# Optimization experiments

Measured on AMD Instinct MI355X. Metric: run time of the kernel, lower is better.

The kernel has to match this reference:

```python
import jax, jax.numpy as jnp
import numpy as np

N = 2048
RESTITUTION = 0.5
EPS = 1e-12


def setup_inputs() -> dict:
    key = jax.random.key(0)
    k1, k2, k3, k4 = jax.random.split(key, 4)
    pos = jax.random.uniform(k1, (N, 2), jnp.float32, 0.0, 200.0)
    rad = jax.random.uniform(k2, (N,), jnp.float32, 0.5, 2.0)
    vel = jax.random.normal(k3, (N, 2), jnp.float32)
    mass = jax.random.uniform(k4, (N,), jnp.float32, 0.5, 2.0)
    return {"pos": pos, "rad": rad, "vel": vel, "mass": mass, "seed": 0}


def _forward(pos, rad, vel, mass, seed):
    rkey = jax.random.key(seed)
    skey = jax.random.split(rkey)[0]  # mirrors skey = jr.split(rkey)[0]
    # ---- pairwise circle-vs-circle contact tests, lower triangle i > j ----
    d = pos[:, None, :] - pos[None, :, :]            # [N,N,2], vector j -> i
    dist = jnp.sqrt(jnp.sum(d * d, -1) + EPS)        # [N,N]
    pen = (rad[:, None] + rad[None, :]) - dist       # penetration depth
    tri = jnp.arange(N)[:, None] > jnp.arange(N)[None, :]
    valid = (pen > 0.0) & tri                        # i < j pairs are nan'd in original
    normal = d / dist[..., None]
    pen_vec_raw = normal * pen[..., None]            # [N,N,2]
    cp_raw = 0.5 * (pos[:, None, :] + pos[None, :, :])  # contact point (midpoint)
    # scatter counts of non-nan contacts (computed in original, unused downstream)
    counts = valid.astype(jnp.int32)
    # ---- bernoulli(0.5)-gated recording into all_contacts ----
    skey = jax.random.split(skey)[0]
    gkey, _ = jax.random.split(skey)
    gate = jax.random.bernoulli(gkey, 0.5, (N, N))
    keep = valid & gate
    all_pen = jnp.where(keep[..., None], pen_vec_raw, 0.0)   # init zeros
    all_cp = jnp.where(keep[..., None], cp_raw, jnp.nan)     # init nan
    # ---- per-row uniform random choice among recorded (non-nan) contacts ----
    ok = ~jnp.any(jnp.isnan(all_cp), axis=-1)        # [N,N]
    n_ok = jnp.sum(ok, axis=-1)                      # [N]
    logits = jnp.where(ok, 0.0, -jnp.inf)
    keys = jax.random.split(skey, N)
    sampled = jax.vmap(jax.random.categorical)(keys, logits)  # uniform over valid
    rows = jnp.arange(N)
    chosen_j = jnp.where(n_ok == 0, rows, sampled)   # fall back to self (skipped)
    pen_sel = all_pen[rows, chosen_j]                # [N,2]
    cp_sel = all_cp[rows, chosen_j]                  # [N,2]
    inv_m = 1.0 / mass

    # ---- sequential collision resolution (scatter updates into SoA) ----
    def step(carry, x):
        p, v = carry
        i, j, pv, cp = x
        upd = (i != j) & ~jnp.any(jnp.isnan(cp))
        pi, pj = p[i], p[j]
        vi, vj = v[i], v[j]
        imi, imj = inv_m[i], inv_m[j]
        nrm = pv / (jnp.sqrt(jnp.sum(pv * pv) + EPS))
        corr = pv / (imi + imj)                      # positional de-penetration
        new_pi = pi + corr * imi
        new_pj = pj - corr * imj
        vrel = jnp.dot(vi - vj, nrm)
        jimp = jnp.where(vrel < 0.0, -(1.0 + RESTITUTION) * vrel / (imi + imj), 0.0)
        new_vi = vi + jimp * imi * nrm
        new_vj = vj - jimp * imj * nrm
        p = p.at[i].set(jnp.where(upd, new_pi, pi))
        p = p.at[j].set(jnp.where(upd, new_pj, pj))
        v = v.at[i].set(jnp.where(upd, new_vi, vi))
        v = v.at[j].set(jnp.where(upd, new_vj, vj))
        return (p, v), None

    (pos_out, vel_out), _ = jax.lax.scan(step, (pos, vel), (rows, chosen_j, pen_sel, cp_sel))
    return jnp.concatenate([pos_out, vel_out], axis=-1)  # [N,4]


def reference(pos, rad, vel, mass, seed):
    return _forward(pos, rad, vel, mass, seed)
```

## Files before the change

kernel.cpp:

```cpp
#include <hip/hip_runtime.h>
#include <stdint.h>

#define NPART 2048
#define FEPS 1e-12f
#define PARTITIONABLE 1

__device__ __forceinline__ uint32_t rotl32(uint32_t v, uint32_t r) {
  return (v << r) | (v >> (32u - r));
}

__device__ __forceinline__ void tf2x32(uint32_t k0, uint32_t k1,
                                       uint32_t x0, uint32_t x1,
                                       uint32_t& o0, uint32_t& o1) {
  uint32_t ks2 = k0 ^ k1 ^ 0x1BD11BDAu;
#define TF_RND(r) { x0 += x1; x1 = rotl32(x1, r); x1 ^= x0; }
  x0 += k0; x1 += k1;
  TF_RND(13u) TF_RND(15u) TF_RND(26u) TF_RND(6u)
  x0 += k1; x1 += ks2 + 1u;
  TF_RND(17u) TF_RND(29u) TF_RND(16u) TF_RND(24u)
  x0 += ks2; x1 += k0 + 2u;
  TF_RND(13u) TF_RND(15u) TF_RND(26u) TF_RND(6u)
  x0 += k0; x1 += k1 + 3u;
  TF_RND(17u) TF_RND(29u) TF_RND(16u) TF_RND(24u)
  x0 += k1; x1 += ks2 + 4u;
  TF_RND(13u) TF_RND(15u) TF_RND(26u) TF_RND(6u)
  x0 += ks2; x1 += k0 + 5u;
#undef TF_RND
  o0 = x0; o1 = x1;
}

__device__ __forceinline__ void split_first(uint32_t k0, uint32_t k1,
                                            uint32_t& o0, uint32_t& o1) {
#if PARTITIONABLE
  tf2x32(k0, k1, 0u, 0u, o0, o1);
#else
  uint32_t a0, a1, b0, b1;
  tf2x32(k0, k1, 0u, 2u, a0, a1);
  tf2x32(k0, k1, 1u, 3u, b0, b1);
  o0 = a0; o1 = b0;
#endif
}

__device__ __forceinline__ void split_at(uint32_t k0, uint32_t k1, uint32_t M,
                                         uint32_t r, uint32_t& o0, uint32_t& o1) {
#if PARTITIONABLE
  tf2x32(k0, k1, 0u, r, o0, o1);
#else
  uint32_t c0 = 2u * r, c1 = 2u * r + 1u;
  uint32_t a0, a1;
  if (c0 < M) { tf2x32(k0, k1, c0, c0 + M, a0, a1); o0 = a0; }
  else        { tf2x32(k0, k1, c0 - M, c0, a0, a1); o0 = a1; }
  if (c1 < M) { tf2x32(k0, k1, c1, c1 + M, a0, a1); o1 = a0; }
  else        { tf2x32(k0, k1, c1 - M, c1, a0, a1); o1 = a1; }
#endif
}

__device__ __forceinline__ uint32_t bits_at(uint32_t k0, uint32_t k1,
                                            uint32_t S_half, uint32_t idx) {
  uint32_t a0, a1;
#if PARTITIONABLE
  (void)S_half;
  tf2x32(k0, k1, 0u, idx, a0, a1);
  return a0 ^ a1;
#else
  if (idx < S_half) { tf2x32(k0, k1, idx, idx + S_half, a0, a1); return a0; }
  else              { tf2x32(k0, k1, idx - S_half, idx, a0, a1); return a1; }
#endif
}

__device__ __forceinline__ void derive_keys(int seed, uint32_t& g0, uint32_t& g1,
                                            uint32_t& s0, uint32_t& s1) {
  uint64_t sv = (uint64_t)(int64_t)seed;
  uint32_t k0 = (uint32_t)(sv >> 32), k1 = (uint32_t)sv;
  uint32_t a0, a1;
  split_first(k0, k1, a0, a1);
  split_first(a0, a1, s0, s1);
  split_first(s0, s1, g0, g1);
}

__global__ __launch_bounds__(256) void phase1_choose(
    const float* __restrict__ pos, const float* __restrict__ rad,
    const int* __restrict__ seedp, int* __restrict__ chosen,
    float* __restrict__ pen_out) {
#pragma clang fp contract(off)
  const int lane = threadIdx.x & 63;
  const int i = blockIdx.x + 512 * (threadIdx.x >> 6);

  uint32_t g0, g1, s0, s1;
  derive_keys(seedp[0], g0, g1, s0, s1);
  uint32_t ki0, ki1;
  split_at(s0, s1, (uint32_t)NPART, (uint32_t)i, ki0, ki1);

  const float pix = pos[2 * i], piy = pos[2 * i + 1];
  const float ri = rad[i];

  unsigned long long best = 0ull;
  for (int j = lane; j < i; j += 64) {
    float2 pj = reinterpret_cast<const float2*>(pos)[j];
    float dx = pix - pj.x;
    float dy = piy - pj.y;
    float dist = sqrtf(dx * dx + dy * dy + FEPS);
    float pen = (ri + rad[j]) - dist;
    if (pen > 0.0f) {
      uint32_t gb = bits_at(g0, g1, (uint32_t)NPART * NPART / 2u,
                            (uint32_t)(i * NPART + j));
      if ((gb >> 31) == 0u) {
        uint32_t b = bits_at(ki0, ki1, (uint32_t)NPART / 2u, (uint32_t)j);
        unsigned long long cand =
            ((unsigned long long)(b >> 9) << 32) |
            (uint32_t)(0xFFFFFFFFu - (uint32_t)j);
        if (cand > best) best = cand;
      }
    }
  }
  for (int off = 1; off < 64; off <<= 1) {
    unsigned long long o = __shfl_xor(best, off, 64);
    if (o > best) best = o;
  }
  if (lane == 0) {
    if (best == 0ull) {
      chosen[i] = -1;
      pen_out[2 * i] = 0.0f;
      pen_out[2 * i + 1] = 0.0f;
    } else {
      int j = (int)(0xFFFFFFFFu - (uint32_t)(best & 0xFFFFFFFFu));
      float2 pj = reinterpret_cast<const float2*>(pos)[j];
      float dx = pix - pj.x;
      float dy = piy - pj.y;
      float dist = sqrtf(dx * dx + dy * dy + FEPS);
      float pen = (ri + rad[j]) - dist;
      chosen[i] = j;
      pen_out[2 * i] = (dx / dist) * pen;
      pen_out[2 * i + 1] = (dy / dist) * pen;
    }
  }
}

__global__ __launch_bounds__(256) void phase2_scan(
    const float* __restrict__ pos, const float* __restrict__ vel,
    const float* __restrict__ mass, const int* __restrict__ chosen,
    const float* __restrict__ pen, float* __restrict__ out) {
#pragma clang fp contract(off)
  __shared__ float2 pxy[NPART], vxy[NPART];
  __shared__ int ij[NPART];
  __shared__ float4 PA[NPART];
  __shared__ float4 PB[NPART];
  __shared__ int minK[NPART];
  __shared__ int wsum[4];

  const int tid = threadIdx.x;
  const int lane = tid & 63, w = tid >> 6;

  for (int r = tid; r < NPART; r += 256) {
    pxy[r] = reinterpret_cast<const float2*>(pos)[r];
    vxy[r] = reinterpret_cast<const float2*>(vel)[r];
    minK[r] = 0;
  }

  const int base = tid * 8;
  int4 c0 = reinterpret_cast<const int4*>(chosen)[2 * tid];
  int4 c1 = reinterpret_cast<const int4*>(chosen)[2 * tid + 1];
  int loc[8] = {c0.x, c0.y, c0.z, c0.w, c1.x, c1.y, c1.z, c1.w};
  int c = 0;
#pragma unroll
  for (int t = 0; t < 8; ++t) c += (loc[t] >= 0);

  int incl = c;
#pragma unroll
  for (int off = 1; off < 64; off <<= 1) {
    int v = __shfl_up(incl, off, 64);
    if (lane >= off) incl += v;
  }
  if (lane == 63) wsum[w] = incl;
  __syncthreads();
  int woff = 0, K = 0;
#pragma unroll
  for (int q = 0; q < 4; ++q) {
    int s = wsum[q];
    if (q < w) woff += s;
    K += s;
  }
  {
    int wr = woff + incl - c;
#pragma unroll
    for (int t = 0; t < 8; ++t) {
      if (loc[t] >= 0) { ij[wr] = ((base + t) << 16) | loc[t]; wr++; }
    }
  }
  __syncthreads();

  for (int k = tid; k < K; k += 256) {
    int pr = ij[k];
    int i = pr >> 16, j = pr & 0xFFFF;
    float imi = 1.0f / mass[i];
    float imj = 1.0f / mass[j];
    float s = imi + imj;
    float pvx = pen[2 * i], pvy = pen[2 * i + 1];
    float nn = sqrtf(pvx * pvx + pvy * pvy + FEPS);
    PA[k] = make_float4((pvx / s) * imi, (pvy / s) * imi,
                        (pvx / s) * imj, (pvy / s) * imj);
    PB[k] = make_float4(pvx / nn, pvy / nn, imi, imj);
  }
  __syncthreads();

  int prc[8];
  uint32_t act = 0;
#pragma unroll
  for (int r = 0; r < 8; ++r) {
    int k = r * 256 + tid;
    if (k < K) { prc[r] = ij[k]; act |= (1u << r); }
    else prc[r] = 0;
  }

  for (int round = 1; __syncthreads_or(act != 0); ++round) {
    const int tagbase = round << 12;
#pragma unroll
    for (int r = 0; r < 8; ++r) {
      if (act & (1u << r)) {
        int tag = tagbase | (4095 - (r * 256 + tid));
        atomicMax(&minK[prc[r] >> 16], tag);
        atomicMax(&minK[prc[r] & 0xFFFF], tag);
      }
    }
    __syncthreads();
    int mi[8], mj[8];
#pragma unroll
    for (int r = 0; r < 8; ++r) {
      if (act & (1u << r)) {
        mi[r] = minK[prc[r] >> 16];
        mj[r] = minK[prc[r] & 0xFFFF];
      }
    }
#pragma unroll
    for (int r = 0; r < 8; ++r) {
      if (act & (1u << r)) {
        int k = r * 256 + tid;
        int tag = tagbase | (4095 - k);
        if (mi[r] == tag && mj[r] == tag) {
          int i = prc[r] >> 16, j = prc[r] & 0xFFFF;
          float4 pa = PA[k], pb = PB[k];
          float2 pi = pxy[i], pj = pxy[j];
          pxy[i] = make_float2(pi.x + pa.x, pi.y + pa.y);
          pxy[j] = make_float2(pj.x - pa.z, pj.y - pa.w);
          float2 vi = vxy[i], vj = vxy[j];
          float rx = vi.x - vj.x, ry = vi.y - vj.y;
          float vrel = rx * pb.x + ry * pb.y;
          if (vrel < 0.0f) {
            float s = pb.z + pb.w;
            float jimp = (-1.5f * vrel) / s;
            float ji = jimp * pb.z, jj = jimp * pb.w;
            vxy[i] = make_float2(vi.x + ji * pb.x, vi.y + ji * pb.y);
            vxy[j] = make_float2(vj.x - jj * pb.x, vj.y - jj * pb.y);
          }
          act &= ~(1u << r);
        }
      }
    }
  }

  for (int r = tid; r < NPART; r += 256) {
    float2 p2 = pxy[r], v2 = vxy[r];
    reinterpret_cast<float4*>(out)[r] = make_float4(p2.x, p2.y, v2.x, v2.y);
  }
}

extern "C" void kernel_launch(void* const* d_in, const int* in_sizes, int n_in,
                              void* d_out, int out_size, void* d_ws, size_t ws_size,
                              hipStream_t stream) {
  const float* pos = (const float*)d_in[0];
  const float* rad = (const float*)d_in[1];
  const float* vel = (const float*)d_in[2];
  const float* mass = (const float*)d_in[3];
  const int* seed = (const int*)d_in[4];

  int* chosen = (int*)d_ws;
  float* pen = (float*)((char*)d_ws + NPART * sizeof(int));

  phase1_choose<<<dim3(512), dim3(256), 0, stream>>>(pos, rad, seed, chosen, pen);
  phase2_scan<<<dim3(1), dim3(256), 0, stream>>>(pos, vel, mass, chosen, pen,
                                                 (float*)d_out);
}
```

Baseline: 79.45 us.

## Fire isolated collisions immediately; resolve conflicting pairs in a single wave

Each particle's incidence is counted across the contact pairs. Pairs whose two particles appear in no other pair are applied at once without any round-based conflict resolution. The remaining conflicting pairs are compacted into a list. If that list is small (at most 512), one wavefront resolves it with wave-level sync instead of block-wide barriers each round; otherwise the block-wide tag/atomicMax rounds still run. This cuts the number of block barriers in the sequential scan, at the cost of a prefix-sum compaction and a round cap that could break ordering if exceeded.

```diff
diff --git a/kernel.cpp b/kernel.cpp
--- a/kernel.cpp
+++ b/kernel.cpp
@@ -146,7 +146,8 @@
   __shared__ float4 PA[NPART];
   __shared__ float4 PB[NPART];
   __shared__ int minK[NPART];
-  __shared__ int wsum[4];
+  __shared__ short clist[NPART];
+  __shared__ int wsum[4], wsum2[4];
 
   const int tid = threadIdx.x;
   const int lane = tid & 63, w = tid >> 6;
@@ -200,63 +201,155 @@
     PA[k] = make_float4((pvx / s) * imi, (pvy / s) * imi,
                         (pvx / s) * imj, (pvy / s) * imj);
     PB[k] = make_float4(pvx / nn, pvy / nn, imi, imj);
-  }
-  __syncthreads();
-
-  int prc[8];
-  uint32_t act = 0;
-#pragma unroll
-  for (int r = 0; r < 8; ++r) {
-    int k = r * 256 + tid;
-    if (k < K) { prc[r] = ij[k]; act |= (1u << r); }
-    else prc[r] = 0;
-  }
-
-  for (int round = 1; __syncthreads_or(act != 0); ++round) {
-    const int tagbase = round << 12;
+    atomicAdd(&minK[i], 1);
+    atomicAdd(&minK[j], 1);
+  }
+  __syncthreads();
+
+#define FIRE(kk, ii, jj)                                                 \
+  {                                                                      \
+    float4 pa = PA[kk], pb = PB[kk];                                     \
+    float2 pi = pxy[ii], pj = pxy[jj];                                   \
+    pxy[ii] = make_float2(pi.x + pa.x, pi.y + pa.y);                     \
+    pxy[jj] = make_float2(pj.x - pa.z, pj.y - pa.w);                     \
+    float2 vi = vxy[ii], vj = vxy[jj];                                   \
+    float rx = vi.x - vj.x, ry = vi.y - vj.y;                            \
+    float vrel = rx * pb.x + ry * pb.y;                                  \
+    if (vrel < 0.0f) {                                                   \
+      float sm = pb.z + pb.w;                \
+      float jimp = (-1.5f * vrel) / sm;                                  \
+      float ji = jimp * pb.z, jjm = jimp * pb.w;                         \
+      vxy[ii] = make_float2(vi.x + ji * pb.x, vi.y + ji * pb.y);         \
+      vxy[jj] = make_float2(vj.x - jjm * pb.x, vj.y - jjm * pb.y);       \
+    }                                                                    \
+         \
+  }
+
+  int cfl = 0, cc = 0;
+#pragma unroll
+  for (int t = 0; t < 8; ++t) {
+    int k = base + t;
+    if (k < K) {
+      int pr = ij[k];
+      int i = pr >> 16, j = pr & 0xFFFF;
+      if (minK[i] == 1 && minK[j] == 1) {
+        FIRE(k, i, j);
+      } else {
+        cfl |= (1 << t); cc++;
+      }
+    }
+  }
+  int incl2 = cc;
+#pragma unroll
+  for (int off = 1; off < 64; off <<= 1) {
+    int v = __shfl_up(incl2, off, 64);
+    if (lane >= off) incl2 += v;
+  }
+  if (lane == 63) wsum2[w] = incl2;
+  __syncthreads();
+  int woff2 = 0, Kc = 0;
+#pragma unroll
+  for (int q = 0; q < 4; ++q) {
+    int s = wsum2[q];
+    if (q < w) woff2 += s;
+    Kc += s;
+  }
+  {
+    int wr = woff2 + incl2 - cc;
+#pragma unroll
+    for (int t = 0; t < 8; ++t) {
+      if (cfl & (1 << t)) { clist[wr] = (short)(base + t); wr++; }
+    }
+  }
+  __syncthreads();
+
+  if (Kc <= 512) {
+    if (w == 0) {
+      int prc[8], kkc[8];
+      uint32_t act = 0;
+#pragma unroll
+      for (int r = 0; r < 8; ++r) {
+        int s = r * 64 + lane;
+        if (s < Kc) { kkc[r] = clist[s]; prc[r] = ij[kkc[r]]; act |= (1u << r); }
+        else { kkc[r] = 0; prc[r] = 0; }
+      }
+      for (int round = 1; __any(act); ++round) {
+        const int tagbase = round << 12;
+#pragma unroll
+        for (int r = 0; r < 8; ++r) {
+          if (act & (1u << r)) {
+            int tag = tagbase | (4095 - kkc[r]);
+            atomicMax(&minK[prc[r] >> 16], tag);
+            atomicMax(&minK[prc[r] & 0xFFFF], tag);
+          }
+        }
+        __threadfence_block();
+        int mi[8], mj[8];
+#pragma unroll
+        for (int r = 0; r < 8; ++r) {
+          if (act & (1u << r)) {
+            mi[r] = minK[prc[r] >> 16];
+            mj[r] = minK[prc[r] & 0xFFFF];
+          }
+        }
+#pragma unroll
+        for (int r = 0; r < 8; ++r) {
+          if (act & (1u << r)) {
+            int tag = tagbase | (4095 - kkc[r]);
+            if (mi[r] == tag && mj[r] == tag) {
+              int i = prc[r] >> 16, j = prc[r] & 0xFFFF;
+              FIRE(kkc[r], i, j);
+              act &= ~(1u << r);
+            }
+          }
+        }
+        __threadfence_block();
+        if (round > 4096) break;
+      }
+    }
+  } else {
+    int prc[8], kkc[8];
+    uint32_t act = 0;
 #pragma unroll
     for (int r = 0; r < 8; ++r) {
-      if (act & (1u << r)) {
-        int tag = tagbase | (4095 - (r * 256 + tid));
-        atomicMax(&minK[prc[r] >> 16], tag);
-        atomicMax(&minK[prc[r] & 0xFFFF], tag);
-      }
-    }
-    __syncthreads();
-    int mi[8], mj[8];
-#pragma unroll
-    for (int r = 0; r < 8; ++r) {
-      if (act & (1u << r)) {
-        mi[r] = minK[prc[r] >> 16];
-        mj[r] = minK[prc[r] & 0xFFFF];
-      }
-    }
-#pragma unroll
-    for (int r = 0; r < 8; ++r) {
-      if (act & (1u << r)) {
-        int k = r * 256 + tid;
-        int tag = tagbase | (4095 - k);
-        if (mi[r] == tag && mj[r] == tag) {
-          int i = prc[r] >> 16, j = prc[r] & 0xFFFF;
-          float4 pa = PA[k], pb = PB[k];
-          float2 pi = pxy[i], pj = pxy[j];
-          pxy[i] = make_float2(pi.x + pa.x, pi.y + pa.y);
-          pxy[j] = make_float2(pj.x - pa.z, pj.y - pa.w);
-          float2 vi = vxy[i], vj = vxy[j];
-          float rx = vi.x - vj.x, ry = vi.y - vj.y;
-          float vrel = rx * pb.x + ry * pb.y;
-          if (vrel < 0.0f) {
-            float s = pb.z + pb.w;
-            float jimp = (-1.5f * vrel) / s;
-            float ji = jimp * pb.z, jj = jimp * pb.w;
-            vxy[i] = make_float2(vi.x + ji * pb.x, vi.y + ji * pb.y);
-            vxy[j] = make_float2(vj.x - jj * pb.x, vj.y - jj * pb.y);
+      int s = r * 256 + tid;
+      if (s < Kc) { kkc[r] = clist[s]; prc[r] = ij[kkc[r]]; act |= (1u << r); }
+      else { kkc[r] = 0; prc[r] = 0; }
+    }
+    for (int round = 1; __syncthreads_or(act != 0); ++round) {
+      const int tagbase = round << 12;
+#pragma unroll
+      for (int r = 0; r < 8; ++r) {
+        if (act & (1u << r)) {
+          int tag = tagbase | (4095 - kkc[r]);
+          atomicMax(&minK[prc[r] >> 16], tag);
+          atomicMax(&minK[prc[r] & 0xFFFF], tag);
+        }
+      }
+      __syncthreads();
+      int mi[8], mj[8];
+#pragma unroll
+      for (int r = 0; r < 8; ++r) {
+        if (act & (1u << r)) {
+          mi[r] = minK[prc[r] >> 16];
+          mj[r] = minK[prc[r] & 0xFFFF];
+        }
+      }
+#pragma unroll
+      for (int r = 0; r < 8; ++r) {
+        if (act & (1u << r)) {
+          int tag = tagbase | (4095 - kkc[r]);
+          if (mi[r] == tag && mj[r] == tag) {
+            int i = prc[r] >> 16, j = prc[r] & 0xFFFF;
+            FIRE(kkc[r], i, j);
+            act &= ~(1u << r);
           }
-          act &= ~(1u << r);
-        }
-      }
-    }
-  }
+        }
+      }
+    }
+  }
+#undef FIRE
+  __syncthreads();
 
   for (int r = tid; r < NPART; r += 256) {
     float2 p2 = pxy[r], v2 = vxy[r];
```

New measurement: 82.77 us. +4.2%, slower.
